# Performance work log

Measured on AMD Instinct MI355X. Metric: run time of the kernel, lower is better.

Reference implementation:

```python
import jax, jax.numpy as jnp
import numpy as np

D = 768      # hidden_size
L = 4        # num_hidden_layers
H = 12       # num_attention_heads
I = 3072     # intermediate_size
B, S = 2, 2048
EPS = 1e-5


def setup_inputs() -> dict:
    key = jax.random.key(0)
    ks = jax.random.split(key, 8)
    sc = 0.02
    return {
        "x": jax.random.normal(ks[0], (B, S, D), dtype=jnp.float32),
        # weights stored as [in, out] so y = x @ W + b (same math as torch Linear)
        "qkv_w": jax.random.normal(ks[1], (L, D, 3 * D), dtype=jnp.float32) * sc,
        "qkv_b": jnp.zeros((L, 3 * D), dtype=jnp.float32),
        "out_w": jax.random.normal(ks[2], (L, D, D), dtype=jnp.float32) * sc,
        "out_b": jnp.zeros((L, D), dtype=jnp.float32),
        "ln1_w": jnp.ones((L, D), dtype=jnp.float32),
        "ln1_b": jnp.zeros((L, D), dtype=jnp.float32),
        "fc1_w": jax.random.normal(ks[3], (L, D, I), dtype=jnp.float32) * sc,
        "fc1_b": jnp.zeros((L, I), dtype=jnp.float32),
        "fc2_w": jax.random.normal(ks[4], (L, I, D), dtype=jnp.float32) * sc,
        "fc2_b": jnp.zeros((L, D), dtype=jnp.float32),
        "ln2_w": jnp.ones((L, D), dtype=jnp.float32),
        "ln2_b": jnp.zeros((L, D), dtype=jnp.float32),
    }


def _layer_norm(x, w, b):
    mu = jnp.mean(x, axis=-1, keepdims=True)
    var = jnp.mean(jnp.square(x - mu), axis=-1, keepdims=True)
    return (x - mu) * jax.lax.rsqrt(var + EPS) * w + b


def _encoder(x, qkv_w, qkv_b, out_w, out_b, ln1_w, ln1_b,
             fc1_w, fc1_b, fc2_w, fc2_b, ln2_w, ln2_b):
    hd = D // H
    scale = 1.0 / jnp.sqrt(jnp.float32(hd))

    def block(x, p):
        (qw, qb, ow, ob, l1w, l1b, f1w, f1b, f2w, f2b, l2w, l2b) = p
        # --- attention sub-block (pre-norm residual) ---
        h = _layer_norm(x, l1w, l1b)
        qkv = h @ qw + qb                      # [B,S,3D]
        qkv = qkv.reshape(B, S, H, 3 * hd).transpose(0, 2, 1, 3)  # [B,H,S,3hd]
        q, k, v = jnp.split(qkv, 3, axis=-1)
        logits = jnp.einsum('bhqd,bhkd->bhqk', q, k) * scale       # [B,H,S,S]
        attn = jax.nn.softmax(logits, axis=-1)
        vals = jnp.einsum('bhqk,bhkd->bhqd', attn, v)              # [B,H,S,hd]
        vals = vals.transpose(0, 2, 1, 3).reshape(B, S, D)
        x = x + vals @ ow + ob
        # --- MLP sub-block (pre-norm residual) ---
        h = _layer_norm(x, l2w, l2b)
        h = jax.nn.gelu(h @ f1w + f1b, approximate=False)
        x = x + h @ f2w + f2b
        return x, None

    params = (qkv_w, qkv_b, out_w, out_b, ln1_w, ln1_b,
              fc1_w, fc1_b, fc2_w, fc2_b, ln2_w, ln2_b)
    x, _ = jax.lax.scan(block, x, params)
    return x


def reference(x, qkv_w, qkv_b, out_w, out_b, ln1_w, ln1_b,
              fc1_w, fc1_b, fc2_w, fc2_b, ln2_w, ln2_b):
    return _encoder(x, qkv_w, qkv_b, out_w, out_b, ln1_w, ln1_b,
                    fc1_w, fc1_b, fc2_w, fc2_b, ln2_w, ln2_b)
```

## Files before the change

### kernel.cpp

```cpp
#include <hip/hip_runtime.h>
#include <stdint.h>
#include <math.h>

#define D_MODEL 768
#define NTOK    4096
#define SEQ     2048
#define NHEAD   12
#define HDIM    64
#define D_FF    3072
#define QKV_N   2304

typedef unsigned short ushort_t;
typedef short  sh4    __attribute__((ext_vector_type(4)));
typedef short  short8 __attribute__((ext_vector_type(8)));
typedef float  f32x4  __attribute__((ext_vector_type(4)));
typedef float  f32x16 __attribute__((ext_vector_type(16)));

__device__ __forceinline__ float b2f(ushort_t u) {
  union { unsigned int u; float f; } v; v.u = ((unsigned int)u) << 16; return v.f;
}
__device__ __forceinline__ ushort_t f2b(float f) {
  union { float f; unsigned int u; } v; v.f = f;
  unsigned int u = v.u;
  return (ushort_t)((u + 0x7fffu + ((u >> 16) & 1u)) >> 16);
}
__device__ __forceinline__ unsigned cvtpk_bf16(float lo, float hi) {
  unsigned r;
  asm("v_cvt_pk_bf16_f32 %0, %1, %2" : "=v"(r) : "v"(lo), "v"(hi));
  return r;
}

__global__ __launch_bounds__(256) void transpose_layer(
    const float* __restrict__ qkv_w, const float* __restrict__ out_w,
    const float* __restrict__ fc1_w, const float* __restrict__ fc2_w,
    ushort_t* __restrict__ qkvT, ushort_t* __restrict__ outT,
    ushort_t* __restrict__ f1T, ushort_t* __restrict__ f2T) {
  __shared__ ushort_t tile[32][33];
  int bid = blockIdx.x;
  const float* src; ushort_t* dst; int K, N, tn, tk;
  if (bid < 1728)      { src = qkv_w; dst = qkvT; K = 768;  N = 2304; tn = bid % 72;  tk = bid / 72; }
  else if (bid < 2304) { int b = bid - 1728; src = out_w; dst = outT; K = 768;  N = 768;  tn = b % 24; tk = b / 24; }
  else if (bid < 4608) { int b = bid - 2304; src = fc1_w; dst = f1T;  K = 768;  N = 3072; tn = b % 96; tk = b / 96; }
  else                 { int b = bid - 4608; src = fc2_w; dst = f2T;  K = 3072; N = 768;  tn = b % 24; tk = b / 24; }
  int n0 = tn * 32, k0 = tk * 32;
  int tx = threadIdx.x, ty = threadIdx.y;
  #pragma unroll
  for (int i = 0; i < 32; i += 8)
    tile[ty + i][tx] = f2b(src[(size_t)(k0 + ty + i) * N + n0 + tx]);
  __syncthreads();
  #pragma unroll
  for (int i = 0; i < 32; i += 8)
    dst[(size_t)(n0 + ty + i) * K + k0 + tx] = tile[tx][ty + i];
}

__global__ __launch_bounds__(256) void ln_kernel(const float* __restrict__ x,
                                                 const float* __restrict__ w,
                                                 const float* __restrict__ b,
                                                 ushort_t* __restrict__ out) {
  __shared__ float red[4];
  int tok = blockIdx.x, t = threadIdx.x;
  const float* xr = x + (size_t)tok * D_MODEL;
  float v0 = xr[t], v1 = xr[t + 256], v2 = xr[t + 512];
  float s = v0 + v1 + v2;
  #pragma unroll
  for (int o = 1; o < 64; o <<= 1) s += __shfl_xor(s, o, 64);
  if ((t & 63) == 0) red[t >> 6] = s;
  __syncthreads();
  float mean = (red[0] + red[1] + red[2] + red[3]) * (1.0f / 768.0f);
  __syncthreads();
  float d0 = v0 - mean, d1 = v1 - mean, d2 = v2 - mean;
  float q = d0 * d0 + d1 * d1 + d2 * d2;
  #pragma unroll
  for (int o = 1; o < 64; o <<= 1) q += __shfl_xor(q, o, 64);
  if ((t & 63) == 0) red[t >> 6] = q;
  __syncthreads();
  float var = (red[0] + red[1] + red[2] + red[3]) * (1.0f / 768.0f);
  float rs = rsqrtf(var + 1e-5f);
  ushort_t* orow = out + (size_t)tok * D_MODEL;
  orow[t]       = f2b(d0 * rs * w[t]       + b[t]);
  orow[t + 256] = f2b(d1 * rs * w[t + 256] + b[t + 256]);
  orow[t + 512] = f2b(d2 * rs * w[t + 512] + b[t + 512]);
}

template <int EPI, int TN>
__global__ __launch_bounds__(256) void gemm_kernel(
    const ushort_t* __restrict__ A, const ushort_t* __restrict__ BT,
    const float* __restrict__ bias, const float* __restrict__ resid,
    float* __restrict__ Cf, ushort_t* __restrict__ Cb, int M, int N, int K) {
  constexpr int NI = (TN == 128) ? 4 : 2;
  __shared__ ushort_t As[2][128 * 32];
  __shared__ ushort_t Bs[2][TN * 32];
  int t = threadIdx.x;
  int lane = t & 63, wave = t >> 6;
  int m0 = blockIdx.y * 128, n0 = blockIdx.x * TN;
  int wm = (TN == 128) ? (wave & 1) * 64 : wave * 32;
  int wn = (TN == 128) ? (wave >> 1) * 64 : 0;
  int quad = lane >> 4, l16 = lane & 15;
  int kq = quad * 8;
  int lrow = lane >> 2, lcol = (lane & 3) * 8;

  auto stage = [&](int k0, int buf) {
    #pragma unroll
    for (int c = 0; c < 2; ++c) {
      int rowA = wave * 32 + c * 16 + lrow;
      const ushort_t* ga = A + (size_t)(m0 + rowA) * K + k0 + lcol;
      ushort_t* la = &As[buf][(wave * 32 + c * 16) * 32];
      __builtin_amdgcn_global_load_lds((const __attribute__((address_space(1))) void*)ga,
                                       (__attribute__((address_space(3))) void*)la, 16, 0, 0);
      if (TN == 128 || c == 0) {
        int rowB = (TN == 128) ? rowA : (wave * 16 + lrow);
        const ushort_t* gb = BT + (size_t)(n0 + rowB) * K + k0 + lcol;
        ushort_t* lb = (TN == 128) ? &Bs[buf][(wave * 32 + c * 16) * 32]
                                   : &Bs[buf][(wave * 16) * 32];
        __builtin_amdgcn_global_load_lds((const __attribute__((address_space(1))) void*)gb,
                                         (__attribute__((address_space(3))) void*)lb, 16, 0, 0);
      }
    }
  };

  f32x4 acc[NI][4];
  #pragma unroll
  for (int i = 0; i < NI; ++i)
    #pragma unroll
    for (int j = 0; j < 4; ++j) acc[i][j] = (f32x4){0.f, 0.f, 0.f, 0.f};

  stage(0, 0);
  int nk = K / 32;
  for (int ki = 0; ki < nk; ++ki) {
    int cur = ki & 1;
    __syncthreads();
    if (ki + 1 < nk) stage((ki + 1) * 32, cur ^ 1);
    short8 af[NI], bf[4];
    #pragma unroll
    for (int i = 0; i < NI; ++i)
      af[i] = *(const short8*)&As[cur][(wm + i * 16 + l16) * 32 + kq];
    #pragma unroll
    for (int j = 0; j < 4; ++j)
      bf[j] = *(const short8*)&Bs[cur][(wn + j * 16 + l16) * 32 + kq];
    #pragma unroll
    for (int i = 0; i < NI; ++i)
      #pragma unroll
      for (int j = 0; j < 4; ++j)
        acc[i][j] = __builtin_amdgcn_mfma_f32_16x16x32_bf16(af[i], bf[j], acc[i][j], 0, 0, 0);
  }

  #pragma unroll
  for (int i = 0; i < NI; ++i) {
    #pragma unroll
    for (int j = 0; j < 4; ++j) {
      int col = n0 + wn + j * 16 + l16;
      float bv = bias[col];
      #pragma unroll
      for (int r = 0; r < 4; ++r) {
        int row = m0 + wm + i * 16 + quad * 4 + r;
        float v = acc[i][j][r] + bv;
        if (EPI == 1) v = 0.5f * v * (1.0f + erff(v * 0.70710678118654752f));
        if (EPI == 2) v += resid[(size_t)row * N + col];
        if (EPI == 2) Cf[(size_t)row * N + col] = v;
        else          Cb[(size_t)row * N + col] = f2b(v);
      }
    }
  }
}

__global__ __launch_bounds__(256) void attn_kernel(const ushort_t* __restrict__ qkv,
                                                   ushort_t* __restrict__ out) {
  __shared__ __align__(16) ushort_t Ks[2][64 * 72];
  __shared__ __align__(16) ushort_t Vt[2][64 * 72];
  int t = threadIdx.x;
  int lane = t & 63, wave = t >> 6;
  int l31 = lane & 31, h = lane >> 5, h8 = h * 8;
  int qt = blockIdx.x;
  int bh = blockIdx.y;
  int b = bh / NHEAD, hd = bh % NHEAD;
  size_t base = (size_t)b * SEQ * QKV_N + hd * 192;

  const float kscale = 0.125f * 1.44269504088896f;

  short8 qf[4];
  {
    const ushort_t* qp = qkv + base + (size_t)(qt * 128 + wave * 32 + l31) * QKV_N + h8;
    #pragma unroll
    for (int ks = 0; ks < 4; ++ks) qf[ks] = *(const short8*)(qp + ks * 16);
  }

  int srow = t >> 2, scol = (t & 3) * 16;
  int vrow = t & 63, vblk = wave * 16;
  short8 kr0, kr1, vr0, vr1;
  auto kv_load = [&](int kc) {
    const ushort_t* gk = qkv + base + (size_t)(kc * 64 + srow) * QKV_N + 64 + scol;
    kr0 = *(const short8*)gk;
    kr1 = *(const short8*)(gk + 8);
    const ushort_t* gv = qkv + base + (size_t)(kc * 64 + vrow) * QKV_N + 128 + vblk;
    vr0 = *(const short8*)gv;
    vr1 = *(const short8*)(gv + 8);
  };
  auto kv_write = [&](int buf) {
    *(short8*)&Ks[buf][srow * 72 + scol]     = kr0;
    *(short8*)&Ks[buf][srow * 72 + scol + 8] = kr1;
    #pragma unroll
    for (int e = 0; e < 8; ++e) {
      Vt[buf][(vblk + e) * 72 + vrow]     = (ushort_t)vr0[e];
      Vt[buf][(vblk + 8 + e) * 72 + vrow] = (ushort_t)vr1[e];
    }
  };

  f32x16 o0, o1;
  #pragma unroll
  for (int i = 0; i < 16; ++i) { o0[i] = 0.f; o1[i] = 0.f; }
  float lsum = 0.f;

  kv_load(0);
  kv_write(0);
  int cur = 0;
  for (int kc = 0; kc < SEQ / 64; ++kc) {
    __syncthreads();
    bool more = (kc + 1 < SEQ / 64);
    if (more) kv_load(kc + 1);

    f32x16 s0, s1;
    #pragma unroll
    for (int i = 0; i < 16; ++i) { s0[i] = 0.f; s1[i] = 0.f; }
    __builtin_amdgcn_s_setprio(1);
    #pragma unroll
    for (int ks = 0; ks < 4; ++ks) {
      short8 k0 = *(const short8*)&Ks[cur][(l31)      * 72 + ks * 16 + h8];
      short8 k1 = *(const short8*)&Ks[cur][(32 + l31) * 72 + ks * 16 + h8];
      s0 = __builtin_amdgcn_mfma_f32_32x32x16_bf16(k0, qf[ks], s0, 0, 0, 0);
      s1 = __builtin_amdgcn_mfma_f32_32x32x16_bf16(k1, qf[ks], s1, 0, 0, 0);
    }
    __builtin_amdgcn_s_setprio(0);

    unsigned wpk[2][4][2];
    #pragma unroll
    for (int t2 = 0; t2 < 2; ++t2) {
      #pragma unroll
      for (int g = 0; g < 4; ++g) {
        float p0, p1, p2, p3;
        if (t2 == 0) {
          p0 = exp2f(s0[4 * g + 0] * kscale); p1 = exp2f(s0[4 * g + 1] * kscale);
          p2 = exp2f(s0[4 * g + 2] * kscale); p3 = exp2f(s0[4 * g + 3] * kscale);
        } else {
          p0 = exp2f(s1[4 * g + 0] * kscale); p1 = exp2f(s1[4 * g + 1] * kscale);
          p2 = exp2f(s1[4 * g + 2] * kscale); p3 = exp2f(s1[4 * g + 3] * kscale);
        }
        lsum += (p0 + p1) + (p2 + p3);
        wpk[t2][g][0] = cvtpk_bf16(p0, p1);
        wpk[t2][g][1] = cvtpk_bf16(p2, p3);
      }
    }

    #pragma unroll
    for (int k4 = 0; k4 < 4; ++k4) {
      int t2 = k4 >> 1, j2 = (k4 & 1) * 2;
      unsigned frag[4];
      #pragma unroll
      for (int c = 0; c < 2; ++c) {
        unsigned a  = wpk[t2][j2][c];
        unsigned b2 = wpk[t2][j2 + 1][c];
        unsigned snd = h ? a : b2;
        unsigned rcv = (unsigned)__shfl_xor((int)snd, 32, 64);
        frag[c]     = h ? rcv : a;
        frag[2 + c] = h ? b2 : rcv;
      }
      union { unsigned u[4]; short8 s8; } uc;
      uc.u[0] = frag[0]; uc.u[1] = frag[1]; uc.u[2] = frag[2]; uc.u[3] = frag[3];
      short8 ap = uc.s8;
      short8 v0 = *(const short8*)&Vt[cur][(l31)      * 72 + k4 * 16 + h8];
      short8 v1 = *(const short8*)&Vt[cur][(32 + l31) * 72 + k4 * 16 + h8];
      __builtin_amdgcn_s_setprio(1);
      o0 = __builtin_amdgcn_mfma_f32_32x32x16_bf16(ap, v0, o0, 0, 0, 0);
      o1 = __builtin_amdgcn_mfma_f32_32x32x16_bf16(ap, v1, o1, 0, 0, 0);
      __builtin_amdgcn_s_setprio(0);
    }

    if (more) kv_write(cur ^ 1);
    cur ^= 1;
  }

  lsum += __shfl_xor(lsum, 32, 64);

  size_t obase = (size_t)(b * SEQ + qt * 128 + wave * 32) * D_MODEL + hd * HDIM;
  #pragma unroll
  for (int g = 0; g < 4; ++g) {
    #pragma unroll
    for (int r = 0; r < 4; ++r) {
      int reg = 4 * g + r;
      int qrow = r + 8 * g + 4 * h;
      float inv = 1.0f / __shfl(lsum, qrow, 64);
      ushort_t* orow = out + obase + (size_t)qrow * D_MODEL;
      orow[l31]      = f2b(o0[reg] * inv);
      orow[32 + l31] = f2b(o1[reg] * inv);
    }
  }
}

extern "C" void kernel_launch(void* const* d_in, const int* in_sizes, int n_in,
                              void* d_out, int out_size, void* d_ws, size_t ws_size,
                              hipStream_t stream) {
  const float* x_in  = (const float*)d_in[0];
  const float* qkv_w = (const float*)d_in[1];
  const float* qkv_b = (const float*)d_in[2];
  const float* out_w = (const float*)d_in[3];
  const float* out_b = (const float*)d_in[4];
  const float* ln1_w = (const float*)d_in[5];
  const float* ln1_b = (const float*)d_in[6];
  const float* fc1_w = (const float*)d_in[7];
  const float* fc1_b = (const float*)d_in[8];
  const float* fc2_w = (const float*)d_in[9];
  const float* fc2_b = (const float*)d_in[10];
  const float* ln2_w = (const float*)d_in[11];
  const float* ln2_b = (const float*)d_in[12];

  char* ws = (char*)d_ws;
  size_t off = 0;
  auto alloc = [&](size_t bytes) -> void* {
    void* p = ws + off; off += (bytes + 255) & ~(size_t)255; return p;
  };
  float*    buf_x  = (float*)   alloc((size_t)NTOK * D_MODEL * 4);
  float*    buf_x2 = (float*)   alloc((size_t)NTOK * D_MODEL * 4);
  ushort_t* bigb   = (ushort_t*)alloc((size_t)NTOK * D_FF * 2);
  ushort_t* h_b    = (ushort_t*)alloc((size_t)NTOK * D_MODEL * 2);
  ushort_t* at_b   = (ushort_t*)alloc((size_t)NTOK * D_MODEL * 2);
  ushort_t* qkvT   = (ushort_t*)alloc((size_t)QKV_N * D_MODEL * 2);
  ushort_t* outT   = (ushort_t*)alloc((size_t)D_MODEL * D_MODEL * 2);
  ushort_t* f1T    = (ushort_t*)alloc((size_t)D_FF * D_MODEL * 2);
  ushort_t* f2T    = (ushort_t*)alloc((size_t)D_MODEL * D_FF * 2);

  ushort_t* qkv_a = bigb;
  ushort_t* mlp_b = bigb;

  for (int l = 0; l < 4; ++l) {
    const float* resid_in = (l == 0) ? x_in : buf_x;
    transpose_layer<<<6912, dim3(32, 8), 0, stream>>>(
        qkv_w + (size_t)l * D_MODEL * QKV_N, out_w + (size_t)l * D_MODEL * D_MODEL,
        fc1_w + (size_t)l * D_MODEL * D_FF,  fc2_w + (size_t)l * D_FF * D_MODEL,
        qkvT, outT, f1T, f2T);
    ln_kernel<<<NTOK, 256, 0, stream>>>(resid_in, ln1_w + l * D_MODEL, ln1_b + l * D_MODEL, h_b);
    gemm_kernel<0, 128><<<dim3(QKV_N / 128, NTOK / 128), 256, 0, stream>>>(
        h_b, qkvT, qkv_b + l * QKV_N, nullptr, nullptr, qkv_a, NTOK, QKV_N, D_MODEL);
    attn_kernel<<<dim3(SEQ / 128, 2 * NHEAD), 256, 0, stream>>>(qkv_a, at_b);
    gemm_kernel<2, 64><<<dim3(D_MODEL / 64, NTOK / 128), 256, 0, stream>>>(
        at_b, outT, out_b + l * D_MODEL, resid_in, buf_x2, nullptr, NTOK, D_MODEL, D_MODEL);
    ln_kernel<<<NTOK, 256, 0, stream>>>(buf_x2, ln2_w + l * D_MODEL, ln2_b + l * D_MODEL, h_b);
    gemm_kernel<1, 128><<<dim3(D_FF / 128, NTOK / 128), 256, 0, stream>>>(
        h_b, f1T, fc1_b + l * D_FF, nullptr, nullptr, mlp_b, NTOK, D_FF, D_MODEL);
    float* x_next = (l < 3) ? buf_x : (float*)d_out;
    gemm_kernel<2, 64><<<dim3(D_MODEL / 64, NTOK / 128), 256, 0, stream>>>(
        mlp_b, f2T, fc2_b + l * D_MODEL, buf_x2, x_next, nullptr, NTOK, D_MODEL, D_FF);
  }
  (void)in_sizes; (void)n_in; (void)out_size; (void)ws_size;
}
```

Baseline: 1.048 ms.

## Split attention KV range across wave pairs with smaller query tiles

The attention kernel now handles 64 query rows per block instead of 128. Each pair of waves processes alternating 64-key chunks of the KV sequence, and the partial outputs and row sums are merged through shared memory at the end. This doubles the grid size to improve occupancy and latency hiding, and the launch bounds now request 3 blocks per CU. The V transpose store is also changed to write packed 32-bit pairs. The cost is twice the K/V global traffic per query, an extra reduction step with a barrier, and more registers for double-buffered loads.

```diff
diff --git a/kernel.cpp b/kernel.cpp
--- a/kernel.cpp
+++ b/kernel.cpp
@@ -163,13 +163,15 @@
   }
 }
 
-__global__ __launch_bounds__(256) void attn_kernel(const ushort_t* __restrict__ qkv,
-                                                   ushort_t* __restrict__ out) {
+__global__ __launch_bounds__(256, 3) void attn_kernel(const ushort_t* __restrict__ qkv,
+                                                      ushort_t* __restrict__ out) {
   __shared__ __align__(16) ushort_t Ks[2][64 * 72];
   __shared__ __align__(16) ushort_t Vt[2][64 * 72];
   int t = threadIdx.x;
   int lane = t & 63, wave = t >> 6;
   int l31 = lane & 31, h = lane >> 5, h8 = h * 8;
+  int pair = wave >> 1;
+  int wq = wave & 1;
   int qt = blockIdx.x;
   int bh = blockIdx.y;
   int b = bh / NHEAD, hd = bh % NHEAD;
@@ -179,29 +181,31 @@
 
   short8 qf[4];
   {
-    const ushort_t* qp = qkv + base + (size_t)(qt * 128 + wave * 32 + l31) * QKV_N + h8;
+    const ushort_t* qp = qkv + base + (size_t)(qt * 64 + wq * 32 + l31) * QKV_N + h8;
     #pragma unroll
     for (int ks = 0; ks < 4; ++ks) qf[ks] = *(const short8*)(qp + ks * 16);
   }
 
   int srow = t >> 2, scol = (t & 3) * 16;
-  int vrow = t & 63, vblk = wave * 16;
-  short8 kr0, kr1, vr0, vr1;
-  auto kv_load = [&](int kc) {
-    const ushort_t* gk = qkv + base + (size_t)(kc * 64 + srow) * QKV_N + 64 + scol;
-    kr0 = *(const short8*)gk;
-    kr1 = *(const short8*)(gk + 8);
-    const ushort_t* gv = qkv + base + (size_t)(kc * 64 + vrow) * QKV_N + 128 + vblk;
-    vr0 = *(const short8*)gv;
-    vr1 = *(const short8*)(gv + 8);
+  int vk = (t & 31) * 2, vd = (t >> 5) * 8;
+  short8 krA[2], krB[2], vrA[2], vrB[2];
+  auto kv_load = [&](int c, int p) {
+    const ushort_t* gk = qkv + base + (size_t)(c * 64 + srow) * QKV_N + 64 + scol;
+    krA[p] = *(const short8*)gk;
+    krB[p] = *(const short8*)(gk + 8);
+    const ushort_t* gv = qkv + base + (size_t)(c * 64 + vk) * QKV_N + 128 + vd;
+    vrA[p] = *(const short8*)gv;
+    vrB[p] = *(const short8*)(gv + QKV_N);
   };
-  auto kv_write = [&](int buf) {
-    *(short8*)&Ks[buf][srow * 72 + scol]     = kr0;
-    *(short8*)&Ks[buf][srow * 72 + scol + 8] = kr1;
+  auto kv_write = [&](int p) {
+    *(short8*)&Ks[p][srow * 72 + scol]     = krA[p];
+    *(short8*)&Ks[p][srow * 72 + scol + 8] = krB[p];
+    unsigned* vtw = (unsigned*)&Vt[p][0];
     #pragma unroll
     for (int e = 0; e < 8; ++e) {
-      Vt[buf][(vblk + e) * 72 + vrow]     = (ushort_t)vr0[e];
-      Vt[buf][(vblk + 8 + e) * 72 + vrow] = (ushort_t)vr1[e];
+      unsigned pk = (unsigned)(unsigned short)vrA[p][e] |
+                    ((unsigned)(unsigned short)vrB[p][e] << 16);
+      vtw[(vd + e) * 36 + (vk >> 1)] = pk;
     }
   };
 
@@ -210,13 +214,16 @@
   for (int i = 0; i < 16; ++i) { o0[i] = 0.f; o1[i] = 0.f; }
   float lsum = 0.f;
 
-  kv_load(0);
-  kv_write(0);
-  int cur = 0;
-  for (int kc = 0; kc < SEQ / 64; ++kc) {
+  kv_load(0, 0);
+  kv_load(1, 1);
+  for (int it = 0; it < SEQ / 128; ++it) {
+    kv_write(0);
+    kv_write(1);
     __syncthreads();
-    bool more = (kc + 1 < SEQ / 64);
-    if (more) kv_load(kc + 1);
+    if (it + 1 < SEQ / 128) {
+      kv_load(2 * it + 2, 0);
+      kv_load(2 * it + 3, 1);
+    }
 
     f32x16 s0, s1;
     #pragma unroll
@@ -224,8 +231,8 @@
     __builtin_amdgcn_s_setprio(1);
     #pragma unroll
     for (int ks = 0; ks < 4; ++ks) {
-      short8 k0 = *(const short8*)&Ks[cur][(l31)      * 72 + ks * 16 + h8];
-      short8 k1 = *(const short8*)&Ks[cur][(32 + l31) * 72 + ks * 16 + h8];
+      short8 k0 = *(const short8*)&Ks[pair][(l31)      * 72 + ks * 16 + h8];
+      short8 k1 = *(const short8*)&Ks[pair][(32 + l31) * 72 + ks * 16 + h8];
       s0 = __builtin_amdgcn_mfma_f32_32x32x16_bf16(k0, qf[ks], s0, 0, 0, 0);
       s1 = __builtin_amdgcn_mfma_f32_32x32x16_bf16(k1, qf[ks], s1, 0, 0, 0);
     }
@@ -266,31 +273,43 @@
       union { unsigned u[4]; short8 s8; } uc;
       uc.u[0] = frag[0]; uc.u[1] = frag[1]; uc.u[2] = frag[2]; uc.u[3] = frag[3];
       short8 ap = uc.s8;
-      short8 v0 = *(const short8*)&Vt[cur][(l31)      * 72 + k4 * 16 + h8];
-      short8 v1 = *(const short8*)&Vt[cur][(32 + l31) * 72 + k4 * 16 + h8];
+      short8 v0 = *(const short8*)&Vt[pair][(l31)      * 72 + k4 * 16 + h8];
+      short8 v1 = *(const short8*)&Vt[pair][(32 + l31) * 72 + k4 * 16 + h8];
       __builtin_amdgcn_s_setprio(1);
       o0 = __builtin_amdgcn_mfma_f32_32x32x16_bf16(ap, v0, o0, 0, 0, 0);
       o1 = __builtin_amdgcn_mfma_f32_32x32x16_bf16(ap, v1, o1, 0, 0, 0);
       __builtin_amdgcn_s_setprio(0);
     }
-
-    if (more) kv_write(cur ^ 1);
-    cur ^= 1;
-  }
-
-  lsum += __shfl_xor(lsum, 32, 64);
-
-  size_t obase = (size_t)(b * SEQ + qt * 128 + wave * 32) * D_MODEL + hd * HDIM;
-  #pragma unroll
-  for (int g = 0; g < 4; ++g) {
-    #pragma unroll
-    for (int r = 0; r < 4; ++r) {
-      int reg = 4 * g + r;
-      int qrow = r + 8 * g + 4 * h;
-      float inv = 1.0f / __shfl(lsum, qrow, 64);
-      ushort_t* orow = out + obase + (size_t)qrow * D_MODEL;
-      orow[l31]      = f2b(o0[reg] * inv);
-      orow[32 + l31] = f2b(o1[reg] * inv);
+    __syncthreads();
+  }
+
+  float* cb = (float*)&Ks[0][0];
+  if (wave >= 2) {
+    int slot = ((wave - 2) * 64 + lane) * 33;
+    #pragma unroll
+    for (int i = 0; i < 16; ++i) { cb[slot + i] = o0[i]; cb[slot + 16 + i] = o1[i]; }
+    cb[slot + 32] = lsum;
+  }
+  __syncthreads();
+  if (wave < 2) {
+    int slot = (wave * 64 + lane) * 33;
+    #pragma unroll
+    for (int i = 0; i < 16; ++i) { o0[i] += cb[slot + i]; o1[i] += cb[slot + 16 + i]; }
+    lsum += cb[slot + 32];
+    lsum += __shfl_xor(lsum, 32, 64);
+
+    size_t obase = (size_t)(b * SEQ + qt * 64 + wave * 32) * D_MODEL + hd * HDIM;
+    #pragma unroll
+    for (int g = 0; g < 4; ++g) {
+      #pragma unroll
+      for (int r = 0; r < 4; ++r) {
+        int reg = 4 * g + r;
+        int qrow = r + 8 * g + 4 * h;
+        float inv = 1.0f / __shfl(lsum, qrow, 64);
+        ushort_t* orow = out + obase + (size_t)qrow * D_MODEL;
+        orow[l31]      = f2b(o0[reg] * inv);
+        orow[32 + l31] = f2b(o1[reg] * inv);
+      }
     }
   }
 }
@@ -339,7 +358,7 @@
     ln_kernel<<<NTOK, 256, 0, stream>>>(resid_in, ln1_w + l * D_MODEL, ln1_b + l * D_MODEL, h_b);
     gemm_kernel<0, 128><<<dim3(QKV_N / 128, NTOK / 128), 256, 0, stream>>>(
         h_b, qkvT, qkv_b + l * QKV_N, nullptr, nullptr, qkv_a, NTOK, QKV_N, D_MODEL);
-    attn_kernel<<<dim3(SEQ / 128, 2 * NHEAD), 256, 0, stream>>>(qkv_a, at_b);
+    attn_kernel<<<dim3(SEQ / 64, 2 * NHEAD), 256, 0, stream>>>(qkv_a, at_b);
     gemm_kernel<2, 64><<<dim3(D_MODEL / 64, NTOK / 128), 256, 0, stream>>>(
         at_b, outT, out_b + l * D_MODEL, resid_in, buf_x2, nullptr, NTOK, D_MODEL, D_MODEL);
     ln_kernel<<<NTOK, 256, 0, stream>>>(buf_x2, ln2_w + l * D_MODEL, ln2_b + l * D_MODEL, h_b);
```

New measurement: 987.6 us. -5.8%, faster.

## Split attention keys across wave pairs and remap GEMM tiles per XCD

Applied to the files above, without the earlier changes.

The attention kernel now processes 64 query rows per block, with two wave pairs each taking half of every 128-key chunk. Partial outputs and row sums are combined through LDS at the end. This doubles the grid, raises the occupancy hint, and packs V transposes into 32-bit LDS stores. Separately, GEMM block IDs are remapped so consecutive tiles land on the same XCD for better L2 reuse. The cost is an extra LDS reduction and an extra sync per chunk.

```diff
diff --git a/kernel.cpp b/kernel.cpp
--- a/kernel.cpp
+++ b/kernel.cpp
@@ -11,7 +11,6 @@
 #define QKV_N   2304
 
 typedef unsigned short ushort_t;
-typedef short  sh4    __attribute__((ext_vector_type(4)));
 typedef short  short8 __attribute__((ext_vector_type(8)));
 typedef float  f32x4  __attribute__((ext_vector_type(4)));
 typedef float  f32x16 __attribute__((ext_vector_type(16)));
@@ -92,7 +91,13 @@
   __shared__ ushort_t Bs[2][TN * 32];
   int t = threadIdx.x;
   int lane = t & 63, wave = t >> 6;
-  int m0 = blockIdx.y * 128, n0 = blockIdx.x * TN;
+  int gx = gridDim.x;
+  int nwg = gx * gridDim.y;
+  int bid0 = blockIdx.y * gx + blockIdx.x;
+  int qn = nwg >> 3, rm = nwg & 7;
+  int xcd = bid0 & 7, pos = bid0 >> 3;
+  int wg = (xcd < rm ? xcd * (qn + 1) : rm * (qn + 1) + (xcd - rm) * qn) + pos;
+  int m0 = (wg / gx) * 128, n0 = (wg % gx) * TN;
   int wm = (TN == 128) ? (wave & 1) * 64 : wave * 32;
   int wn = (TN == 128) ? (wave >> 1) * 64 : 0;
   int quad = lane >> 4, l16 = lane & 15;
@@ -163,13 +168,15 @@
   }
 }
 
-__global__ __launch_bounds__(256) void attn_kernel(const ushort_t* __restrict__ qkv,
-                                                   ushort_t* __restrict__ out) {
+__global__ __launch_bounds__(256, 3) void attn_kernel(const ushort_t* __restrict__ qkv,
+                                                      ushort_t* __restrict__ out) {
   __shared__ __align__(16) ushort_t Ks[2][64 * 72];
   __shared__ __align__(16) ushort_t Vt[2][64 * 72];
   int t = threadIdx.x;
   int lane = t & 63, wave = t >> 6;
   int l31 = lane & 31, h = lane >> 5, h8 = h * 8;
+  int kh = wave & 1, qh = wave >> 1;
+  int kw = kh * 32;
   int qt = blockIdx.x;
   int bh = blockIdx.y;
   int b = bh / NHEAD, hd = bh % NHEAD;
@@ -179,118 +186,127 @@
 
   short8 qf[4];
   {
-    const ushort_t* qp = qkv + base + (size_t)(qt * 128 + wave * 32 + l31) * QKV_N + h8;
+    const ushort_t* qp = qkv + base + (size_t)(qt * 64 + qh * 32 + l31) * QKV_N + h8;
     #pragma unroll
     for (int ks = 0; ks < 4; ++ks) qf[ks] = *(const short8*)(qp + ks * 16);
   }
 
-  int srow = t >> 2, scol = (t & 3) * 16;
-  int vrow = t & 63, vblk = wave * 16;
-  short8 kr0, kr1, vr0, vr1;
-  auto kv_load = [&](int kc) {
-    const ushort_t* gk = qkv + base + (size_t)(kc * 64 + srow) * QKV_N + 64 + scol;
-    kr0 = *(const short8*)gk;
-    kr1 = *(const short8*)(gk + 8);
-    const ushort_t* gv = qkv + base + (size_t)(kc * 64 + vrow) * QKV_N + 128 + vblk;
-    vr0 = *(const short8*)gv;
-    vr1 = *(const short8*)(gv + 8);
+  int krow = t >> 1, kcol = (t & 1) * 32;
+  int kcb = krow >> 6, krl = krow & 63;
+  int kp = t & 63, vdb = (t >> 6) * 16;
+  int vcb = kp >> 5, kpl = kp & 31;
+  short8 kr[4], va[2], vb[2];
+  auto kv_load = [&](int sbase) {
+    const ushort_t* gk = qkv + base + (size_t)(sbase + krow) * QKV_N + 64 + kcol;
+    #pragma unroll
+    for (int i = 0; i < 4; ++i) kr[i] = *(const short8*)(gk + i * 8);
+    const ushort_t* gv = qkv + base + (size_t)(sbase + 2 * kp) * QKV_N + 128 + vdb;
+    va[0] = *(const short8*)gv;           va[1] = *(const short8*)(gv + 8);
+    vb[0] = *(const short8*)(gv + QKV_N); vb[1] = *(const short8*)(gv + QKV_N + 8);
   };
-  auto kv_write = [&](int buf) {
-    *(short8*)&Ks[buf][srow * 72 + scol]     = kr0;
-    *(short8*)&Ks[buf][srow * 72 + scol + 8] = kr1;
-    #pragma unroll
-    for (int e = 0; e < 8; ++e) {
-      Vt[buf][(vblk + e) * 72 + vrow]     = (ushort_t)vr0[e];
-      Vt[buf][(vblk + 8 + e) * 72 + vrow] = (ushort_t)vr1[e];
+  auto kv_write = [&]() {
+    #pragma unroll
+    for (int i = 0; i < 4; ++i)
+      *(short8*)&Ks[kcb][krl * 72 + kcol + i * 8] = kr[i];
+    unsigned* vtw = (unsigned*)&Vt[vcb][0];
+    #pragma unroll
+    for (int half = 0; half < 2; ++half)
+      #pragma unroll
+      for (int e = 0; e < 8; ++e) {
+        unsigned pk = (unsigned)(unsigned short)va[half][e] |
+                      ((unsigned)(unsigned short)vb[half][e] << 16);
+        vtw[(vdb + half * 8 + e) * 36 + kpl] = pk;
+      }
+  };
+
+  f32x16 o0, o1;
+  #pragma unroll
+  for (int i = 0; i < 16; ++i) { o0[i] = 0.f; o1[i] = 0.f; }
+  float ls = 0.f;
+
+  kv_load(0);
+  for (int it = 0; it < SEQ / 128; ++it) {
+    kv_write();
+    __syncthreads();
+    if (it + 1 < SEQ / 128) kv_load((it + 1) * 128);
+
+    #pragma unroll
+    for (int c = 0; c < 2; ++c) {
+      f32x16 s;
+      #pragma unroll
+      for (int i = 0; i < 16; ++i) s[i] = 0.f;
+      __builtin_amdgcn_s_setprio(1);
+      #pragma unroll
+      for (int ks = 0; ks < 4; ++ks) {
+        short8 kf = *(const short8*)&Ks[c][(kw + l31) * 72 + ks * 16 + h8];
+        s = __builtin_amdgcn_mfma_f32_32x32x16_bf16(kf, qf[ks], s, 0, 0, 0);
+      }
+      __builtin_amdgcn_s_setprio(0);
+
+      unsigned wpk[4][2];
+      #pragma unroll
+      for (int g = 0; g < 4; ++g) {
+        float p0 = exp2f(s[4 * g + 0] * kscale), p1 = exp2f(s[4 * g + 1] * kscale);
+        float p2 = exp2f(s[4 * g + 2] * kscale), p3 = exp2f(s[4 * g + 3] * kscale);
+        ls += (p0 + p1) + (p2 + p3);
+        wpk[g][0] = cvtpk_bf16(p0, p1);
+        wpk[g][1] = cvtpk_bf16(p2, p3);
+      }
+
+      #pragma unroll
+      for (int k4 = 0; k4 < 2; ++k4) {
+        int j2 = k4 * 2;
+        unsigned f[4];
+        #pragma unroll
+        for (int c2 = 0; c2 < 2; ++c2) {
+          unsigned a  = wpk[j2][c2];
+          unsigned b2 = wpk[j2 + 1][c2];
+          unsigned snd = h ? a : b2;
+          unsigned rcv = (unsigned)__shfl_xor((int)snd, 32, 64);
+          f[c2]     = h ? rcv : a;
+          f[2 + c2] = h ? b2 : rcv;
+        }
+        union { unsigned u[4]; short8 s8; } uc;
+        uc.u[0] = f[0]; uc.u[1] = f[1]; uc.u[2] = f[2]; uc.u[3] = f[3];
+        short8 ap = uc.s8;
+        short8 v0 = *(const short8*)&Vt[c][(l31)      * 72 + kw + k4 * 16 + h8];
+        short8 v1 = *(const short8*)&Vt[c][(32 + l31) * 72 + kw + k4 * 16 + h8];
+        __builtin_amdgcn_s_setprio(1);
+        o0 = __builtin_amdgcn_mfma_f32_32x32x16_bf16(ap, v0, o0, 0, 0, 0);
+        o1 = __builtin_amdgcn_mfma_f32_32x32x16_bf16(ap, v1, o1, 0, 0, 0);
+        __builtin_amdgcn_s_setprio(0);
+      }
     }
-  };
-
-  f32x16 o0, o1;
-  #pragma unroll
-  for (int i = 0; i < 16; ++i) { o0[i] = 0.f; o1[i] = 0.f; }
-  float lsum = 0.f;
-
-  kv_load(0);
-  kv_write(0);
-  int cur = 0;
-  for (int kc = 0; kc < SEQ / 64; ++kc) {
     __syncthreads();
-    bool more = (kc + 1 < SEQ / 64);
-    if (more) kv_load(kc + 1);
-
-    f32x16 s0, s1;
-    #pragma unroll
-    for (int i = 0; i < 16; ++i) { s0[i] = 0.f; s1[i] = 0.f; }
-    __builtin_amdgcn_s_setprio(1);
-    #pragma unroll
-    for (int ks = 0; ks < 4; ++ks) {
-      short8 k0 = *(const short8*)&Ks[cur][(l31)      * 72 + ks * 16 + h8];
-      short8 k1 = *(const short8*)&Ks[cur][(32 + l31) * 72 + ks * 16 + h8];
-      s0 = __builtin_amdgcn_mfma_f32_32x32x16_bf16(k0, qf[ks], s0, 0, 0, 0);
-      s1 = __builtin_amdgcn_mfma_f32_32x32x16_bf16(k1, qf[ks], s1, 0, 0, 0);
-    }
-    __builtin_amdgcn_s_setprio(0);
-
-    unsigned wpk[2][4][2];
-    #pragma unroll
-    for (int t2 = 0; t2 < 2; ++t2) {
-      #pragma unroll
-      for (int g = 0; g < 4; ++g) {
-        float p0, p1, p2, p3;
-        if (t2 == 0) {
-          p0 = exp2f(s0[4 * g + 0] * kscale); p1 = exp2f(s0[4 * g + 1] * kscale);
-          p2 = exp2f(s0[4 * g + 2] * kscale); p3 = exp2f(s0[4 * g + 3] * kscale);
-        } else {
-          p0 = exp2f(s1[4 * g + 0] * kscale); p1 = exp2f(s1[4 * g + 1] * kscale);
-          p2 = exp2f(s1[4 * g + 2] * kscale); p3 = exp2f(s1[4 * g + 3] * kscale);
-        }
-        lsum += (p0 + p1) + (p2 + p3);
-        wpk[t2][g][0] = cvtpk_bf16(p0, p1);
-        wpk[t2][g][1] = cvtpk_bf16(p2, p3);
-      }
-    }
-
-    #pragma unroll
-    for (int k4 = 0; k4 < 4; ++k4) {
-      int t2 = k4 >> 1, j2 = (k4 & 1) * 2;
-      unsigned frag[4];
-      #pragma unroll
-      for (int c = 0; c < 2; ++c) {
-        unsigned a  = wpk[t2][j2][c];
-        unsigned b2 = wpk[t2][j2 + 1][c];
-        unsigned snd = h ? a : b2;
-        unsigned rcv = (unsigned)__shfl_xor((int)snd, 32, 64);
-        frag[c]     = h ? rcv : a;
-        frag[2 + c] = h ? b2 : rcv;
-      }
-      union { unsigned u[4]; short8 s8; } uc;
-      uc.u[0] = frag[0]; uc.u[1] = frag[1]; uc.u[2] = frag[2]; uc.u[3] = frag[3];
-      short8 ap = uc.s8;
-      short8 v0 = *(const short8*)&Vt[cur][(l31)      * 72 + k4 * 16 + h8];
-      short8 v1 = *(const short8*)&Vt[cur][(32 + l31) * 72 + k4 * 16 + h8];
-      __builtin_amdgcn_s_setprio(1);
-      o0 = __builtin_amdgcn_mfma_f32_32x32x16_bf16(ap, v0, o0, 0, 0, 0);
-      o1 = __builtin_amdgcn_mfma_f32_32x32x16_bf16(ap, v1, o1, 0, 0, 0);
-      __builtin_amdgcn_s_setprio(0);
-    }
-
-    if (more) kv_write(cur ^ 1);
-    cur ^= 1;
-  }
-
-  lsum += __shfl_xor(lsum, 32, 64);
-
-  size_t obase = (size_t)(b * SEQ + qt * 128 + wave * 32) * D_MODEL + hd * HDIM;
-  #pragma unroll
-  for (int g = 0; g < 4; ++g) {
-    #pragma unroll
-    for (int r = 0; r < 4; ++r) {
-      int reg = 4 * g + r;
-      int qrow = r + 8 * g + 4 * h;
-      float inv = 1.0f / __shfl(lsum, qrow, 64);
-      ushort_t* orow = out + obase + (size_t)qrow * D_MODEL;
-      orow[l31]      = f2b(o0[reg] * inv);
-      orow[32 + l31] = f2b(o1[reg] * inv);
+  }
+
+  float* slab = (float*)&Ks[0][0];
+  if (kh == 1) {
+    float* s = slab + (size_t)(qh * 64 + lane) * 33;
+    #pragma unroll
+    for (int i = 0; i < 16; ++i) { s[i] = o0[i]; s[16 + i] = o1[i]; }
+    s[32] = ls;
+  }
+  __syncthreads();
+  if (kh == 0) {
+    float* s = slab + (size_t)(qh * 64 + lane) * 33;
+    #pragma unroll
+    for (int i = 0; i < 16; ++i) { o0[i] += s[i]; o1[i] += s[16 + i]; }
+    ls += s[32];
+    ls += __shfl_xor(ls, 32, 64);
+
+    size_t ob = (size_t)(b * SEQ + qt * 64 + qh * 32) * D_MODEL + hd * HDIM;
+    #pragma unroll
+    for (int g = 0; g < 4; ++g) {
+      #pragma unroll
+      for (int r = 0; r < 4; ++r) {
+        int reg = 4 * g + r;
+        int qrow = 8 * g + 4 * h + r;
+        float inv = 1.0f / __shfl(ls, qrow, 64);
+        ushort_t* orow = out + ob + (size_t)qrow * D_MODEL;
+        orow[l31]      = f2b(o0[reg] * inv);
+        orow[32 + l31] = f2b(o1[reg] * inv);
+      }
     }
   }
 }
@@ -339,7 +355,7 @@
     ln_kernel<<<NTOK, 256, 0, stream>>>(resid_in, ln1_w + l * D_MODEL, ln1_b + l * D_MODEL, h_b);
     gemm_kernel<0, 128><<<dim3(QKV_N / 128, NTOK / 128), 256, 0, stream>>>(
         h_b, qkvT, qkv_b + l * QKV_N, nullptr, nullptr, qkv_a, NTOK, QKV_N, D_MODEL);
-    attn_kernel<<<dim3(SEQ / 128, 2 * NHEAD), 256, 0, stream>>>(qkv_a, at_b);
+    attn_kernel<<<dim3(SEQ / 64, 2 * NHEAD), 256, 0, stream>>>(qkv_a, at_b);
     gemm_kernel<2, 64><<<dim3(D_MODEL / 64, NTOK / 128), 256, 0, stream>>>(
         at_b, outT, out_b + l * D_MODEL, resid_in, buf_x2, nullptr, NTOK, D_MODEL, D_MODEL);
     ln_kernel<<<NTOK, 256, 0, stream>>>(buf_x2, ln2_w + l * D_MODEL, ln2_b + l * D_MODEL, h_b);
```

Result: faster. 960.3 us (-8.4%).
